# Kernel optimization log

Measured on AMD Instinct MI355X. Metric: run time of the kernel, lower is better.

The kernel has to match this reference:

```python
import jax, jax.numpy as jnp
import numpy as np

D_STATE = 8
DT_RANK = 8  # ceil(128/16)


def _grouped_1x1(x, w):
    # x: (B,H,W,Cin), w: (g, Cout//g, Cin//g)
    B, H, W, _ = x.shape
    g, o, i = w.shape
    xg = x.reshape(B, H, W, g, i)
    return jnp.einsum('bhwgi,goi->bhwgo', xg, w).reshape(B, H, W, g * o)


def setup_inputs() -> dict:
    key = jax.random.key(0)
    ks = jax.random.split(key, 16)
    B, H, W, C = 8, 64, 64, 128
    g = 4
    D = 128  # expand_dim = d_inner
    N = D_STATE
    R = DT_RANK
    inp = {}
    inp['x'] = jax.random.normal(ks[0], (B, H, W, C), dtype=jnp.float32)
    inp['w1'] = jax.random.normal(ks[1], (g, D // g, C // g), dtype=jnp.float32) * 0.1
    inp['dw'] = jax.random.normal(ks[2], (3, 3, 1, D), dtype=jnp.float32) * 0.1  # HWIO depthwise
    inp['in_proj_w'] = jax.random.normal(ks[3], (2 * D, D), dtype=jnp.float32) * 0.05
    inp['conv1d_w'] = jax.random.normal(ks[4], (D, 3), dtype=jnp.float32) * 0.1
    inp['conv1d_b'] = jax.random.normal(ks[5], (D,), dtype=jnp.float32) * 0.05
    inp['x_proj_w'] = jax.random.normal(ks[6], (R + 2 * N, D), dtype=jnp.float32) * 0.05
    inp['dt_proj_w'] = jax.random.normal(ks[7], (D, R), dtype=jnp.float32) * 0.05
    inp['dt_proj_b'] = jax.random.normal(ks[8], (D,), dtype=jnp.float32) * 0.05
    inp['A_log'] = jnp.log(jnp.tile(jnp.arange(1, N + 1, dtype=jnp.float32)[None, :], (D, 1)))
    inp['D_param'] = jnp.ones((D,), dtype=jnp.float32)
    inp['out_proj_w'] = jax.random.normal(ks[9], (D, D), dtype=jnp.float32) * 0.05
    inp['gamma'] = jnp.ones((D,), dtype=jnp.float32)
    inp['beta'] = jnp.zeros((D,), dtype=jnp.float32)
    inp['w2'] = jax.random.normal(ks[10], (g, D // g, C // g), dtype=jnp.float32) * 0.1
    inp['wout'] = jax.random.normal(ks[11], (g, C // g, D // g), dtype=jnp.float32) * 0.1
    return inp


def _mamba(x_seq, in_proj_w, conv1d_w, conv1d_b, x_proj_w, dt_proj_w, dt_proj_b, A_log, D_param, out_proj_w):
    # x_seq: (B, L, D)
    B, L, D = x_seq.shape
    N, R = D_STATE, DT_RANK
    xz = jnp.einsum('bld,ed->ble', x_seq, in_proj_w)  # (B,L,2D)
    u, z = xz[..., :D], xz[..., D:]
    # causal depthwise conv1d, kernel=3, left pad 2 (torch: padding=2, slice [:L])
    up = jnp.pad(u, ((0, 0), (2, 0), (0, 0)))
    u = (up[:, 0:L] * conv1d_w[:, 0] + up[:, 1:L + 1] * conv1d_w[:, 1]
         + up[:, 2:L + 2] * conv1d_w[:, 2] + conv1d_b)
    u = jax.nn.silu(u)
    x_dbl = jnp.einsum('bld,ed->ble', u, x_proj_w)  # (B,L,R+2N)
    dt = x_dbl[..., :R]
    Bm = x_dbl[..., R:R + N]
    Cm = x_dbl[..., R + N:]
    delta = jax.nn.softplus(jnp.einsum('blr,dr->bld', dt, dt_proj_w) + dt_proj_b)  # (B,L,D)
    A = -jnp.exp(A_log)  # (D,N)

    def step(h, inp):
        d_t, u_t, b_t, c_t = inp  # (B,D),(B,D),(B,N),(B,N)
        dA = jnp.exp(d_t[..., None] * A)            # (B,D,N)
        h = dA * h + (d_t * u_t)[..., None] * b_t[:, None, :]
        y_t = jnp.einsum('bdn,bn->bd', h, c_t)
        return h, y_t

    h0 = jnp.zeros((B, D, N), dtype=x_seq.dtype)
    xs = (jnp.swapaxes(delta, 0, 1), jnp.swapaxes(u, 0, 1),
          jnp.swapaxes(Bm, 0, 1), jnp.swapaxes(Cm, 0, 1))
    _, ys = jax.lax.scan(step, h0, xs)              # ys: (L,B,D)
    y = jnp.swapaxes(ys, 0, 1) + u * D_param
    y = y * jax.nn.silu(z)
    return jnp.einsum('bld,ed->ble', y, out_proj_w)


def reference(x, w1, dw, in_proj_w, conv1d_w, conv1d_b, x_proj_w, dt_proj_w, dt_proj_b,
              A_log, D_param, out_proj_w, gamma, beta, w2, wout):
    B, H, W, C = x.shape
    D = dw.shape[-1]
    x1 = _grouped_1x1(x, w1)  # (B,H,W,D)
    x1 = jax.lax.conv_general_dilated(
        x1, dw, window_strides=(1, 1), padding='SAME',
        feature_group_count=D, dimension_numbers=('NHWC', 'HWIO', 'NHWC'))
    x1 = jax.nn.silu(x1)
    x1_seq = x1.reshape(B, H * W, D)
    x1_seq = _mamba(x1_seq, in_proj_w, conv1d_w, conv1d_b, x_proj_w,
                    dt_proj_w, dt_proj_b, A_log, D_param, out_proj_w)
    x1 = x1_seq.reshape(B, H, W, D)
    mu = jnp.mean(x1, axis=-1, keepdims=True)
    var = jnp.mean(jnp.square(x1 - mu), axis=-1, keepdims=True)
    x1 = (x1 - mu) * jax.lax.rsqrt(var + 1e-5) * gamma + beta
    x2 = jax.nn.silu(_grouped_1x1(x, w2))
    x_fuse = x1 * x2
    return _grouped_1x1(x_fuse, wout)  # (B,H,W,C)
```

## Files before the change

### kernel.cpp

```cpp
#include <hip/hip_runtime.h>
#include <math.h>

#define B_    8
#define C_    128
#define D_    128
#define L_    4096
#define NPOS_ 32768
#define NC_   256
#define S_    16
#define MFL_  1048576

typedef __attribute__((ext_vector_type(8))) short short8;
typedef __attribute__((ext_vector_type(4))) float f32x4;

__device__ __forceinline__ float siluf(float x) { return x / (1.f + __expf(-x)); }
__device__ __forceinline__ float softplusf(float x) {
    if (x > 20.f) return x;
    return __logf(1.f + __expf(x));
}
__device__ __forceinline__ unsigned short f2bf(float f) {
    unsigned int u = __float_as_uint(f);
    u = (u + 0x7FFFu + ((u >> 16) & 1u)) >> 16;
    return (unsigned short)u;
}
__device__ __forceinline__ float bf2f(unsigned short h) {
    return __uint_as_float(((unsigned int)h) << 16);
}
__device__ __forceinline__ void scan_as(float dl, const float* Ar, bool fast, float* a) {
    if (fast) {
        float e1 = __expf(-dl);
        a[0] = e1;
        a[1] = e1 * e1;
        a[2] = a[1] * e1;
        a[3] = a[1] * a[1];
        a[4] = a[3] * e1;
        a[5] = a[3] * a[1];
        a[6] = a[5] * e1;
        a[7] = a[3] * a[3];
    } else {
        #pragma unroll
        for (int n = 0; n < 8; ++n) a[n] = __expf(dl * Ar[n]);
    }
}

__global__ __launch_bounds__(256) void k1_g1x1(const float* __restrict__ x,
                                               const float* __restrict__ w1,
                                               const float* __restrict__ w2,
                                               const float* __restrict__ inW,
                                               const float* __restrict__ OW,
                                               const float* __restrict__ xpw,
                                               unsigned short* __restrict__ inWb,
                                               unsigned short* __restrict__ OWb,
                                               unsigned short* __restrict__ xpwb,
                                               unsigned short* __restrict__ t1b,
                                               unsigned short* __restrict__ x2sb) {
    __shared__ float xs[16 * 128];
    int t = threadIdx.x;
    {
        int i = blockIdx.x * 51 + t;
        if (t < 51 && i < 52224) {
            if (i < 32768)      inWb[i] = f2bf(inW[i]);
            else if (i < 49152) OWb[i - 32768] = f2bf(OW[i - 32768]);
            else                xpwb[i - 49152] = f2bf(xpw[i - 49152]);
        }
    }
    int op = t & 63, ph = t >> 6;
    int g = op >> 4, o2 = (op & 15) * 2;
    const float* w1p = &w1[g * 1024 + o2 * 32];
    const float* w2p = &w2[g * 1024 + o2 * 32];
    float w1r[64], w2r[64];
    #pragma unroll
    for (int i = 0; i < 64; ++i) { w1r[i] = w1p[i]; w2r[i] = w2p[i]; }
    int pos0 = blockIdx.x * 32;
    for (int it = 0; it < 2; ++it) {
        int p0 = pos0 + it * 16;
        #pragma unroll
        for (int q = 0; q < 2; ++q) {
            int fi = t * 2 + q;
            *(float4*)&xs[fi * 4] = *(const float4*)&x[p0 * 128 + fi * 4];
        }
        __syncthreads();
        #pragma unroll
        for (int q = 0; q < 4; ++q) {
            int pl = ph * 4 + q;
            float a1 = 0.f, b1 = 0.f, a2 = 0.f, b2 = 0.f;
            const float* xr = &xs[pl * 128 + g * 32];
            #pragma unroll
            for (int i4 = 0; i4 < 8; ++i4) {
                float4 xv = *(const float4*)&xr[i4 * 4];
                a1 += xv.x * w1r[i4*4]    + xv.y * w1r[i4*4+1]    + xv.z * w1r[i4*4+2]    + xv.w * w1r[i4*4+3];
                b1 += xv.x * w1r[32+i4*4] + xv.y * w1r[32+i4*4+1] + xv.z * w1r[32+i4*4+2] + xv.w * w1r[32+i4*4+3];
                a2 += xv.x * w2r[i4*4]    + xv.y * w2r[i4*4+1]    + xv.z * w2r[i4*4+2]    + xv.w * w2r[i4*4+3];
                b2 += xv.x * w2r[32+i4*4] + xv.y * w2r[32+i4*4+1] + xv.z * w2r[32+i4*4+2] + xv.w * w2r[32+i4*4+3];
            }
            int pos = p0 + pl;
            int db = pos * 128 + g * 32 + o2;
            unsigned int u1 = (unsigned int)f2bf(a1) | ((unsigned int)f2bf(b1) << 16);
            unsigned int u2 = (unsigned int)f2bf(siluf(a2)) | ((unsigned int)f2bf(siluf(b2)) << 16);
            *(unsigned int*)&t1b[db]  = u1;
            *(unsigned int*)&x2sb[db] = u2;
        }
        __syncthreads();
    }
}

__global__ __launch_bounds__(128) void k2_dwconv(const unsigned short* __restrict__ t1b,
                                                 const float* __restrict__ dw,
                                                 unsigned short* __restrict__ x1cb) {
    int d = threadIdx.x;
    float dwr[9];
    #pragma unroll
    for (int k = 0; k < 9; ++k) dwr[k] = dw[k * 128 + d];
    int bid = blockIdx.x;
    int wt = bid & 15, ht = (bid >> 4) & 7, b = bid >> 7;
    int h0 = ht * 8, w0 = wt * 4;
    float rows[10][6];
    #pragma unroll
    for (int r = 0; r < 10; ++r) {
        int hh = h0 - 1 + r;
        bool hv = (hh >= 0) && (hh < 64);
        #pragma unroll
        for (int c = 0; c < 6; ++c) {
            int w = w0 - 1 + c;
            bool wvv = (w >= 0) && (w < 64);
            rows[r][c] = (hv && wvv) ? bf2f(t1b[((b * 64 + hh) * 64 + w) * 128 + d]) : 0.f;
        }
    }
    #pragma unroll
    for (int hi = 0; hi < 8; ++hi) {
        #pragma unroll
        for (int wi = 0; wi < 4; ++wi) {
            float acc = rows[hi][wi]     * dwr[0] + rows[hi][wi+1]   * dwr[1] + rows[hi][wi+2]   * dwr[2]
                      + rows[hi+1][wi]   * dwr[3] + rows[hi+1][wi+1] * dwr[4] + rows[hi+1][wi+2] * dwr[5]
                      + rows[hi+2][wi]   * dwr[6] + rows[hi+2][wi+1] * dwr[7] + rows[hi+2][wi+2] * dwr[8];
            x1cb[((b * 64 + h0 + hi) * 64 + w0 + wi) * 128 + d] = f2bf(siluf(acc));
        }
    }
}

__global__ __launch_bounds__(256) void k3_mfma(const unsigned short* __restrict__ Abf,
                                               const unsigned short* __restrict__ Bbf,
                                               unsigned short* __restrict__ urawb,
                                               unsigned short* __restrict__ zb) {
    __shared__ unsigned short Al[64 * 72];
    __shared__ unsigned short Bl[128 * 72];
    int t = threadIdx.x;
    int pos0 = (blockIdx.x >> 1) * 64;
    int half = blockIdx.x & 1;
    const unsigned short* Bh = Bbf + (size_t)half * 128 * 128;
    unsigned short* dst = half ? zb : urawb;
    int lane = t & 63, wv = t >> 6;
    int lanem = lane & 15, laneq = lane >> 4;
    f32x4 acc[8];
    #pragma unroll
    for (int i = 0; i < 8; ++i) acc[i] = (f32x4){0.f, 0.f, 0.f, 0.f};
    for (int kc = 0; kc < 2; ++kc) {
        #pragma unroll
        for (int q = 0; q < 2; ++q) {
            int c = t + q * 256;
            int row = c >> 3, col = c & 7;
            *(int4*)&Al[row * 72 + col * 8] = *(const int4*)&Abf[(pos0 + row) * 128 + kc * 64 + col * 8];
        }
        #pragma unroll
        for (int q = 0; q < 4; ++q) {
            int c = t + q * 256;
            int row = c >> 3, col = c & 7;
            *(int4*)&Bl[row * 72 + col * 8] = *(const int4*)&Bh[row * 128 + kc * 64 + col * 8];
        }
        __syncthreads();
        #pragma unroll
        for (int ks = 0; ks < 2; ++ks) {
            short8 af = *(const short8*)&Al[(wv * 16 + lanem) * 72 + ks * 32 + laneq * 8];
            #pragma unroll
            for (int ni = 0; ni < 8; ++ni) {
                short8 bfr = *(const short8*)&Bl[(ni * 16 + lanem) * 72 + ks * 32 + laneq * 8];
                acc[ni] = __builtin_amdgcn_mfma_f32_16x16x32_bf16(af, bfr, acc[ni], 0, 0, 0);
            }
        }
        __syncthreads();
    }
    #pragma unroll
    for (int ni = 0; ni < 8; ++ni)
        #pragma unroll
        for (int r = 0; r < 4; ++r) {
            int m = pos0 + wv * 16 + laneq * 4 + r;
            int n = ni * 16 + lanem;
            dst[m * 128 + n] = f2bf(acc[ni][r]);
        }
}

__global__ __launch_bounds__(256) void k45_convproj(const unsigned short* __restrict__ urawb,
                                                    const float* __restrict__ cw,
                                                    const float* __restrict__ cb,
                                                    const unsigned short* __restrict__ xpwb,
                                                    const float* __restrict__ dtw,
                                                    const float* __restrict__ dtb,
                                                    const float* __restrict__ A_log,
                                                    unsigned short* __restrict__ usb,
                                                    unsigned short* __restrict__ deltab,
                                                    float* __restrict__ Bm,
                                                    float* __restrict__ Cm,
                                                    float* __restrict__ cA,
                                                    float* __restrict__ cB) {
    __shared__ unsigned short uA[32 * 136];
    __shared__ unsigned short xB[32 * 136];
    __shared__ float xdb[32 * 36];
    int t = threadIdx.x;
    int d = t & 127, ph = t >> 7;
    for (int i = t; i < 32 * 128; i += 256) {
        int n = i >> 7, k = i & 127;
        xB[n * 136 + k] = (n < 24) ? xpwb[n * 128 + k] : (unsigned short)0;
    }
    float cw0 = cw[d * 3 + 0], cw1 = cw[d * 3 + 1], cw2 = cw[d * 3 + 2], cbr = cb[d];
    float dtwr[8];
    #pragma unroll
    for (int r = 0; r < 8; ++r) dtwr[r] = dtw[d * 8 + r];
    float dtbr = dtb[d];
    float Ar[8]; bool fast = true;
    #pragma unroll
    for (int n = 0; n < 8; ++n) {
        Ar[n] = -__expf(A_log[d * 8 + n]);
        fast = fast && (fabsf(Ar[n] + (float)(n + 1)) < 2e-3f);
    }

    int gpos0 = blockIdx.x * 32;
    int ll0 = (gpos0 & 4095) + ph * 16;
    int base = (gpos0 + ph * 16) * 128 + d;
    float ur0 = (ll0 >= 2) ? bf2f(urawb[base - 256]) : 0.f;
    float ur1 = (ll0 >= 1) ? bf2f(urawb[base - 128]) : 0.f;
    #pragma unroll
    for (int q = 0; q < 16; ++q) {
        float urq = bf2f(urawb[base + q * 128]);
        float v = siluf(ur0 * cw0 + ur1 * cw1 + urq * cw2 + cbr);
        unsigned short vb = f2bf(v);
        usb[base + q * 128] = vb;
        uA[(ph * 16 + q) * 136 + d] = vb;
        ur0 = ur1; ur1 = urq;
    }
    __syncthreads();
    int lane = t & 63, wv = t >> 6;
    int lanem = lane & 15, laneq = lane >> 4;
    int m0 = (wv & 1) * 16, n0 = (wv >> 1) * 16;
    f32x4 accx = (f32x4){0.f, 0.f, 0.f, 0.f};
    #pragma unroll
    for (int ks = 0; ks < 4; ++ks) {
        short8 af  = *(const short8*)&uA[(m0 + lanem) * 136 + ks * 32 + laneq * 8];
        short8 bfr = *(const short8*)&xB[(n0 + lanem) * 136 + ks * 32 + laneq * 8];
        accx = __builtin_amdgcn_mfma_f32_16x16x32_bf16(af, bfr, accx, 0, 0, 0);
    }
    #pragma unroll
    for (int r = 0; r < 4; ++r)
        xdb[(m0 + laneq * 4 + r) * 36 + n0 + lanem] = accx[r];
    __syncthreads();
    float h[8], ap[8];
    #pragma unroll
    for (int n = 0; n < 8; ++n) { h[n] = 0.f; ap[n] = 1.f; }
    #pragma unroll
    for (int q = 0; q < 16; ++q) {
        int pl = ph * 16 + q;
        const float* xrow = &xdb[pl * 36];
        float4 d0 = *(const float4*)&xrow[0];
        float4 d1 = *(const float4*)&xrow[4];
        float dt = dtbr + d0.x * dtwr[0] + d0.y * dtwr[1] + d0.z * dtwr[2] + d0.w * dtwr[3]
                        + d1.x * dtwr[4] + d1.y * dtwr[5] + d1.z * dtwr[6] + d1.w * dtwr[7];
        unsigned short dlb = f2bf(softplusf(dt));
        deltab[base + q * 128] = dlb;
        float dl = bf2f(dlb);
        float du = dl * bf2f(uA[pl * 136 + d]);
        float bmv[8];
        *(float4*)&bmv[0] = *(const float4*)&xrow[8];
        *(float4*)&bmv[4] = *(const float4*)&xrow[12];
        float a[8];
        scan_as(dl, Ar, fast, a);
        #pragma unroll
        for (int n = 0; n < 8; ++n) {
            ap[n] *= a[n];
            h[n] = a[n] * h[n] + du * bmv[n];
        }
    }
    int bH = gpos0 >> 12;
    int c  = ((gpos0 & 4095) >> 4) + ph;
    int obase = ((bH * NC_ + c) * 128 + d) * 8;
    *(float4*)&cA[obase]     = make_float4(ap[0], ap[1], ap[2], ap[3]);
    *(float4*)&cA[obase + 4] = make_float4(ap[4], ap[5], ap[6], ap[7]);
    *(float4*)&cB[obase]     = make_float4(h[0], h[1], h[2], h[3]);
    *(float4*)&cB[obase + 4] = make_float4(h[4], h[5], h[6], h[7]);
    if (t < 128) {
        int p = t >> 2, q = t & 3;
        float4 v = *(const float4*)&xdb[p * 36 + 8 + q * 4];
        int gp = gpos0 + p;
        if (q < 2) *(float4*)&Bm[gp * 8 + q * 4] = v;
        else       *(float4*)&Cm[gp * 8 + (q - 2) * 4] = v;
    }
}

__global__ __launch_bounds__(256) void k6a_scan(float* __restrict__ cA,
                                                float* __restrict__ cB,
                                                float* __restrict__ AgA,
                                                float* __restrict__ AgB) {
    int id = blockIdx.x * 256 + threadIdx.x;
    int dn = id & 1023;
    int grp = (id >> 10) & 15;
    int b = id >> 14;
    float Apre = 1.f, h = 0.f;
    int base = (b * NC_ + grp * 16) * 1024 + dn;
    #pragma unroll 4
    for (int j = 0; j < 16; ++j) {
        int idx = base + j * 1024;
        float a  = cA[idx];
        float bv = cB[idx];
        cA[idx] = Apre;
        cB[idx] = h;
        Apre *= a;
        h = a * h + bv;
    }
    int aidx = (b * 16 + grp) * 1024 + dn;
    AgA[aidx] = Apre;
    AgB[aidx] = h;
}

__global__ __launch_bounds__(256) void k6b_scan(const float* __restrict__ AgA,
                                                const float* __restrict__ AgB,
                                                float* __restrict__ gcar) {
    int id = blockIdx.x * 256 + threadIdx.x;
    int dn = id & 1023;
    int b = id >> 10;
    float h = 0.f;
    #pragma unroll
    for (int grp = 0; grp < 16; ++grp) {
        int idx = (b * 16 + grp) * 1024 + dn;
        float Ag = AgA[idx];
        float Bg = AgB[idx];
        gcar[idx] = h;
        h = Ag * h + Bg;
    }
}

__global__ __launch_bounds__(256) void k7f_fused(const unsigned short* __restrict__ deltab,
                                                 const unsigned short* __restrict__ usb,
                                                 const float* __restrict__ Bm,
                                                 const float* __restrict__ Cm,
                                                 const unsigned short* __restrict__ zb,
                                                 const float* __restrict__ A_log,
                                                 const float* __restrict__ Dp,
                                                 const float* __restrict__ Apre,
                                                 const float* __restrict__ Bpre,
                                                 const float* __restrict__ gcar,
                                                 const unsigned short* __restrict__ OWb,
                                                 const float* __restrict__ gamma,
                                                 const float* __restrict__ beta,
                                                 const unsigned short* __restrict__ x2sb,
                                                 const float* __restrict__ wout,
                                                 float* __restrict__ out) {
    __shared__ __align__(16) char smem[37888];
    unsigned short* yA = (unsigned short*)smem;
    unsigned short* Bl = (unsigned short*)(smem + 18432);
    float* xz = (float*)smem;
    __shared__ float woutL[4 * 1160];
    __shared__ float gbL[256];
    int t = threadIdx.x;
    for (int idx = t; idx < 4096; idx += 256) {
        int g = idx >> 10, r = idx & 1023, o = r >> 5, i = r & 31;
        woutL[g * 1160 + o * 36 + i] = wout[idx];
    }
    if (t < 128) gbL[t] = gamma[t];
    else         gbL[t] = beta[t - 128];

    int d = t & 127, ph = t >> 7;
    int b = blockIdx.x >> 6, cblk = blockIdx.x & 63;
    float Ar[8]; bool fast = true;
    #pragma unroll
    for (int n = 0; n < 8; ++n) {
        Ar[n] = -__expf(A_log[d * 8 + n]);
        fast = fast && (fabsf(Ar[n] + (float)(n + 1)) < 2e-3f);
    }
    float Dpr = Dp[d];
    int ybase = (d >> 6) * (64 * 72) + (d & 63);
    for (int cc = 0; cc < 2; ++cc) {
        int cl = ph * 2 + cc;
        int c = cblk * 4 + cl;
        int cbase = ((b * NC_ + c) * 128 + d) * 8;
        float4 ap0 = *(const float4*)&Apre[cbase];
        float4 ap1 = *(const float4*)&Apre[cbase + 4];
        float4 bp0 = *(const float4*)&Bpre[cbase];
        float4 bp1 = *(const float4*)&Bpre[cbase + 4];
        int gbase = (b * 16 + (c >> 4)) * 1024 + d * 8;
        float4 g0 = *(const float4*)&gcar[gbase];
        float4 g1 = *(const float4*)&gcar[gbase + 4];
        float h[8] = { fmaf(g0.x, ap0.x, bp0.x), fmaf(g0.y, ap0.y, bp0.y),
                       fmaf(g0.z, ap0.z, bp0.z), fmaf(g0.w, ap0.w, bp0.w),
                       fmaf(g1.x, ap1.x, bp1.x), fmaf(g1.y, ap1.y, bp1.y),
                       fmaf(g1.z, ap1.z, bp1.z), fmaf(g1.w, ap1.w, bp1.w) };
        int base  = (b * L_ + c * S_) * 128 + d;
        int bbase = (b * L_ + c * S_) * 8;
        #pragma unroll
        for (int s = 0; s < S_; ++s) {
            float dl = bf2f(deltab[base + s * 128]);
            float uv = bf2f(usb[base + s * 128]);
            float zv = bf2f(zb[base + s * 128]);
            float du = dl * uv;
            float4 bm0 = *(const float4*)&Bm[bbase + s * 8];
            float4 bm1 = *(const float4*)&Bm[bbase + s * 8 + 4];
            float4 cm0 = *(const float4*)&Cm[bbase + s * 8];
            float4 cm1 = *(const float4*)&Cm[bbase + s * 8 + 4];
            float a[8];
            scan_as(dl, Ar, fast, a);
            h[0] = a[0] * h[0] + du * bm0.x;
            h[1] = a[1] * h[1] + du * bm0.y;
            h[2] = a[2] * h[2] + du * bm0.z;
            h[3] = a[3] * h[3] + du * bm0.w;
            h[4] = a[4] * h[4] + du * bm1.x;
            h[5] = a[5] * h[5] + du * bm1.y;
            h[6] = a[6] * h[6] + du * bm1.z;
            h[7] = a[7] * h[7] + du * bm1.w;
            float yv = h[0] * cm0.x + h[1] * cm0.y + h[2] * cm0.z + h[3] * cm0.w
                     + h[4] * cm1.x + h[5] * cm1.y + h[6] * cm1.z + h[7] * cm1.w;
            yv = (yv + uv * Dpr) * siluf(zv);
            yA[ybase + (cl * 16 + s) * 72] = f2bf(yv);
        }
    }
    __syncthreads();

    int lane = t & 63, wv = t >> 6;
    int lanem = lane & 15, laneq = lane >> 4;
    f32x4 acc[8];
    #pragma unroll
    for (int i = 0; i < 8; ++i) acc[i] = (f32x4){0.f, 0.f, 0.f, 0.f};
    for (int kc = 0; kc < 2; ++kc) {
        #pragma unroll
        for (int q = 0; q < 4; ++q) {
            int cidx = t + q * 256;
            int row = cidx >> 3, col = cidx & 7;
            *(int4*)&Bl[row * 72 + col * 8] = *(const int4*)&OWb[row * 128 + kc * 64 + col * 8];
        }
        __syncthreads();
        #pragma unroll
        for (int ks = 0; ks < 2; ++ks) {
            short8 af = *(const short8*)&yA[kc * (64 * 72) + (wv * 16 + lanem) * 72 + ks * 32 + laneq * 8];
            #pragma unroll
            for (int ni = 0; ni < 8; ++ni) {
                short8 bfr = *(const short8*)&Bl[(ni * 16 + lanem) * 72 + ks * 32 + laneq * 8];
                acc[ni] = __builtin_amdgcn_mfma_f32_16x16x32_bf16(af, bfr, acc[ni], 0, 0, 0);
            }
        }
        __syncthreads();
    }
    #pragma unroll
    for (int ni = 0; ni < 8; ++ni) {
        int ch = ni * 16 + lanem;
        int col = ch + ((ch >> 5) << 2);
        #pragma unroll
        for (int r = 0; r < 4; ++r)
            xz[(wv * 16 + laneq * 4 + r) * 148 + col] = bf2f(f2bf(acc[ni][r]));
    }
    __syncthreads();

    int g = t & 3, pos = t >> 2;
    int gpos = b * L_ + cblk * 64 + pos;
    const float* xrow0 = &xz[pos * 148 + g * 36];
    float v[32];
    #pragma unroll
    for (int i4 = 0; i4 < 8; ++i4) {
        float4 xv = *(const float4*)&xrow0[i4 * 4];
        v[i4*4+0] = xv.x; v[i4*4+1] = xv.y;
        v[i4*4+2] = xv.z; v[i4*4+3] = xv.w;
    }
    float s = 0.f, s2 = 0.f;
    #pragma unroll
    for (int i = 0; i < 32; ++i) { s += v[i]; s2 += v[i] * v[i]; }
    s  += __shfl_xor(s, 1, 64);  s  += __shfl_xor(s, 2, 64);
    s2 += __shfl_xor(s2, 1, 64); s2 += __shfl_xor(s2, 2, 64);
    float m = s * (1.f / 128.f);
    float var = s2 * (1.f / 128.f) - m * m;
    float rstd = rsqrtf(var + 1e-5f);
    #pragma unroll
    for (int i4 = 0; i4 < 8; ++i4) {
        ushort4 xv = *(const ushort4*)&x2sb[gpos * 128 + g * 32 + i4 * 4];
        unsigned short xa[4] = {xv.x, xv.y, xv.z, xv.w};
        #pragma unroll
        for (int k = 0; k < 4; ++k) {
            int e = g * 32 + i4 * 4 + k;
            float vv = (v[i4 * 4 + k] - m) * rstd * gbL[e] + gbL[128 + e];
            v[i4 * 4 + k] = vv * bf2f(xa[k]);
        }
    }

    const float* wg = &woutL[g * 1160];
    int obase = gpos * 128 + g * 32;
    #pragma unroll
    for (int ob = 0; ob < 8; ++ob) {
        float o4[4];
        #pragma unroll
        for (int oo = 0; oo < 4; ++oo) {
            int o = ob * 4 + oo;
            float acc2 = 0.f;
            #pragma unroll
            for (int i4 = 0; i4 < 8; ++i4) {
                float4 wv4 = *(const float4*)&wg[o * 36 + i4 * 4];
                acc2 += v[i4*4] * wv4.x + v[i4*4+1] * wv4.y
                      + v[i4*4+2] * wv4.z + v[i4*4+3] * wv4.w;
            }
            o4[oo] = acc2;
        }
        *(float4*)&out[obase + ob * 4] = make_float4(o4[0], o4[1], o4[2], o4[3]);
    }
}

extern "C" void kernel_launch(void* const* d_in, const int* in_sizes, int n_in,
                              void* d_out, int out_size, void* d_ws, size_t ws_size,
                              hipStream_t stream) {
    (void)in_sizes; (void)n_in; (void)out_size; (void)ws_size;
    const float* x         = (const float*)d_in[0];
    const float* w1        = (const float*)d_in[1];
    const float* dw        = (const float*)d_in[2];
    const float* in_proj_w = (const float*)d_in[3];
    const float* conv1d_w  = (const float*)d_in[4];
    const float* conv1d_b  = (const float*)d_in[5];
    const float* x_proj_w  = (const float*)d_in[6];
    const float* dt_proj_w = (const float*)d_in[7];
    const float* dt_proj_b = (const float*)d_in[8];
    const float* A_log     = (const float*)d_in[9];
    const float* D_param   = (const float*)d_in[10];
    const float* out_proj_w= (const float*)d_in[11];
    const float* gamma     = (const float*)d_in[12];
    const float* beta      = (const float*)d_in[13];
    const float* w2        = (const float*)d_in[14];
    const float* wout      = (const float*)d_in[15];
    float* out = (float*)d_out;

    float* ws = (float*)d_ws;
    unsigned short* x2sb   = (unsigned short*)(ws);
    unsigned short* t1b    = (unsigned short*)(ws + 2  * (size_t)MFL_);
    unsigned short* x1cb   = (unsigned short*)(ws + 4  * (size_t)MFL_);
    unsigned short* urawb  = (unsigned short*)(ws + 6  * (size_t)MFL_);
    unsigned short* zb     = (unsigned short*)(ws + 8  * (size_t)MFL_);
    unsigned short* usb    = (unsigned short*)(ws + 14 * (size_t)MFL_);
    unsigned short* deltab = (unsigned short*)(ws + 16 * (size_t)MFL_);
    float* Bm    = ws + 18 * (size_t)MFL_;
    float* Cm    = Bm + (size_t)NPOS_ * 8;
    float* cA    = Cm + (size_t)NPOS_ * 8;
    float* cB    = cA + 2 * (size_t)MFL_;
    float* scanw = cB + 2 * (size_t)MFL_;
    float* AgA   = scanw;
    float* AgB   = scanw + 131072;
    float* gcar  = scanw + 262144;
    unsigned short* inWb = (unsigned short*)(scanw + 2 * (size_t)MFL_);
    unsigned short* OWb  = inWb + 32768;
    unsigned short* xpwb = OWb + 16384;

    k1_g1x1<<<1024, 256, 0, stream>>>(x, w1, w2, in_proj_w, out_proj_w, x_proj_w,
                                      inWb, OWb, xpwb, t1b, x2sb);
    k2_dwconv<<<1024, 128, 0, stream>>>(t1b, dw, x1cb);
    k3_mfma<<<1024, 256, 0, stream>>>(x1cb, inWb, urawb, zb);
    k45_convproj<<<1024, 256, 0, stream>>>(urawb, conv1d_w, conv1d_b, xpwb,
                                           dt_proj_w, dt_proj_b, A_log,
                                           usb, deltab, Bm, Cm, cA, cB);
    k6a_scan<<<512, 256, 0, stream>>>(cA, cB, AgA, AgB);
    k6b_scan<<<32, 256, 0, stream>>>(AgA, AgB, gcar);
    k7f_fused<<<512, 256, 0, stream>>>(deltab, usb, Bm, Cm, zb, A_log, D_param,
                                       cA, cB, gcar, OWb, gamma, beta, x2sb, wout, out);
}
```

Baseline: 214.9 us.

## Fuse all seven stages into one persistent kernel with software grid barriers

```diff
diff --git a/kernel.cpp b/kernel.cpp
--- a/kernel.cpp
+++ b/kernel.cpp
@@ -9,6 +9,7 @@
 #define NC_   256
 #define S_    16
 #define MFL_  1048576
+#define NBLK_ 512u
 
 typedef __attribute__((ext_vector_type(8))) short short8;
 typedef __attribute__((ext_vector_type(4))) float f32x4;
@@ -43,466 +44,496 @@
     }
 }
 
-__global__ __launch_bounds__(256) void k1_g1x1(const float* __restrict__ x,
-                                               const float* __restrict__ w1,
-                                               const float* __restrict__ w2,
-                                               const float* __restrict__ inW,
-                                               const float* __restrict__ OW,
-                                               const float* __restrict__ xpw,
-                                               unsigned short* __restrict__ inWb,
-                                               unsigned short* __restrict__ OWb,
-                                               unsigned short* __restrict__ xpwb,
-                                               unsigned short* __restrict__ t1b,
-                                               unsigned short* __restrict__ x2sb) {
-    __shared__ float xs[16 * 128];
+__device__ __forceinline__ void gbar(unsigned int* bar, int phase) {
+    __syncthreads();
+    if (threadIdx.x == 0) {
+        unsigned int* c = bar + phase * 16;
+        __threadfence();
+        __hip_atomic_fetch_add(&c[blockIdx.x & 7], 1u, __ATOMIC_ACQ_REL, __HIP_MEMORY_SCOPE_AGENT);
+        if (blockIdx.x == 0) {
+            unsigned int s;
+            do {
+                __builtin_amdgcn_s_sleep(1);
+                s = 0;
+                #pragma unroll
+                for (int i = 0; i < 8; ++i)
+                    s += __hip_atomic_load(&c[i], __ATOMIC_RELAXED, __HIP_MEMORY_SCOPE_AGENT);
+            } while (s < NBLK_);
+            __hip_atomic_store(&c[8], 1u, __ATOMIC_RELEASE, __HIP_MEMORY_SCOPE_AGENT);
+        } else {
+            while (__hip_atomic_load(&c[8], __ATOMIC_ACQUIRE, __HIP_MEMORY_SCOPE_AGENT) == 0u)
+                __builtin_amdgcn_s_sleep(1);
+        }
+        __threadfence();
+    }
+    __syncthreads();
+}
+
+__global__ __launch_bounds__(256, 2) void mega(
+        const float* __restrict__ x,
+        const float* __restrict__ w1,
+        const float* __restrict__ w2,
+        const float* __restrict__ inW,
+        const float* __restrict__ OW,
+        const float* __restrict__ xpw,
+        const float* __restrict__ dw,
+        const float* __restrict__ cw,
+        const float* __restrict__ cb,
+        const float* __restrict__ dtw,
+        const float* __restrict__ dtb,
+        const float* __restrict__ A_log,
+        const float* __restrict__ Dp,
+        const float* __restrict__ gamma,
+        const float* __restrict__ beta,
+        const float* __restrict__ wout,
+        unsigned short* __restrict__ inWb,
+        unsigned short* __restrict__ OWb,
+        unsigned short* __restrict__ xpwb,
+        unsigned short* __restrict__ t1b,
+        unsigned short* __restrict__ x2sb,
+        unsigned short* __restrict__ x1cb,
+        unsigned short* __restrict__ urawb,
+        unsigned short* __restrict__ zb,
+        unsigned short* __restrict__ usb,
+        unsigned short* __restrict__ deltab,
+        float* __restrict__ Bm,
+        float* __restrict__ Cm,
+        float* __restrict__ cA,
+        float* __restrict__ cB,
+        float* __restrict__ AgA,
+        float* __restrict__ AgB,
+        float* __restrict__ gcar,
+        float* __restrict__ out,
+        unsigned int* __restrict__ bar) {
+    __shared__ __align__(16) char arena[57472];
     int t = threadIdx.x;
-    {
-        int i = blockIdx.x * 51 + t;
-        if (t < 51 && i < 52224) {
-            if (i < 32768)      inWb[i] = f2bf(inW[i]);
-            else if (i < 49152) OWb[i - 32768] = f2bf(OW[i - 32768]);
-            else                xpwb[i - 49152] = f2bf(xpw[i - 49152]);
-        }
-    }
-    int op = t & 63, ph = t >> 6;
-    int g = op >> 4, o2 = (op & 15) * 2;
-    const float* w1p = &w1[g * 1024 + o2 * 32];
-    const float* w2p = &w2[g * 1024 + o2 * 32];
-    float w1r[64], w2r[64];
-    #pragma unroll
-    for (int i = 0; i < 64; ++i) { w1r[i] = w1p[i]; w2r[i] = w2p[i]; }
-    int pos0 = blockIdx.x * 32;
-    for (int it = 0; it < 2; ++it) {
-        int p0 = pos0 + it * 16;
-        #pragma unroll
-        for (int q = 0; q < 2; ++q) {
-            int fi = t * 2 + q;
-            *(float4*)&xs[fi * 4] = *(const float4*)&x[p0 * 128 + fi * 4];
+
+    {
+        float* xs = (float*)arena;
+        for (int it2 = 0; it2 < 2; ++it2) {
+            int obid = (int)blockIdx.x + it2 * 512;
+            int i = obid * 51 + t;
+            if (t < 51 && i < 52224) {
+                if (i < 32768)      inWb[i] = f2bf(inW[i]);
+                else if (i < 49152) OWb[i - 32768] = f2bf(OW[i - 32768]);
+                else                xpwb[i - 49152] = f2bf(xpw[i - 49152]);
+            }
+        }
+        int op = t & 63, ph = t >> 6;
+        int g = op >> 4, o2 = (op & 15) * 2;
+        const float* w1p = &w1[g * 1024 + o2 * 32];
+        const float* w2p = &w2[g * 1024 + o2 * 32];
+        float w1r[64], w2r[64];
+        #pragma unroll
+        for (int i = 0; i < 64; ++i) { w1r[i] = w1p[i]; w2r[i] = w2p[i]; }
+        for (int it2 = 0; it2 < 2; ++it2) {
+            int obid = (int)blockIdx.x + it2 * 512;
+            int pos0 = obid * 32;
+            for (int it = 0; it < 2; ++it) {
+                int p0 = pos0 + it * 16;
+                #pragma unroll
+                for (int q = 0; q < 2; ++q) {
+                    int fi = t * 2 + q;
+                    *(float4*)&xs[fi * 4] = *(const float4*)&x[p0 * 128 + fi * 4];
+                }
+                __syncthreads();
+                #pragma unroll
+                for (int q = 0; q < 4; ++q) {
+                    int pl = ph * 4 + q;
+                    float a1 = 0.f, b1 = 0.f, a2 = 0.f, b2 = 0.f;
+                    const float* xr = &xs[pl * 128 + g * 32];
+                    #pragma unroll
+                    for (int i4 = 0; i4 < 8; ++i4) {
+                        float4 xv = *(const float4*)&xr[i4 * 4];
+                        a1 += xv.x * w1r[i4*4]    + xv.y * w1r[i4*4+1]    + xv.z * w1r[i4*4+2]    + xv.w * w1r[i4*4+3];
+                        b1 += xv.x * w1r[32+i4*4] + xv.y * w1r[32+i4*4+1] + xv.z * w1r[32+i4*4+2] + xv.w * w1r[32+i4*4+3];
+                        a2 += xv.x * w2r[i4*4]    + xv.y * w2r[i4*4+1]    + xv.z * w2r[i4*4+2]    + xv.w * w2r[i4*4+3];
+                        b2 += xv.x * w2r[32+i4*4] + xv.y * w2r[32+i4*4+1] + xv.z * w2r[32+i4*4+2] + xv.w * w2r[32+i4*4+3];
+                    }
+                    int pos = p0 + pl;
+                    int db = pos * 128 + g * 32 + o2;
+                    unsigned int u1 = (unsigned int)f2bf(a1) | ((unsigned int)f2bf(b1) << 16);
+                    unsigned int u2 = (unsigned int)f2bf(siluf(a2)) | ((unsigned int)f2bf(siluf(b2)) << 16);
+                    *(unsigned int*)&t1b[db]  = u1;
+                    *(unsigned int*)&x2sb[db] = u2;
+                }
+                __syncthreads();
+            }
+        }
+    }
+    gbar(bar, 0);
+
+    {
+        int obid = (int)blockIdx.x * 2 + (t >> 7);
+        int d = t & 127;
+        float dwr[9];
+        #pragma unroll
+        for (int k = 0; k < 9; ++k) dwr[k] = dw[k * 128 + d];
+        int wt = obid & 15, ht = (obid >> 4) & 7, b = obid >> 7;
+        int h0 = ht * 8, w0 = wt * 4;
+        float rows[10][6];
+        #pragma unroll
+        for (int r = 0; r < 10; ++r) {
+            int hh = h0 - 1 + r;
+            bool hv = (hh >= 0) && (hh < 64);
+            #pragma unroll
+            for (int c = 0; c < 6; ++c) {
+                int w = w0 - 1 + c;
+                bool wvv = (w >= 0) && (w < 64);
+                rows[r][c] = (hv && wvv) ? bf2f(t1b[((b * 64 + hh) * 64 + w) * 128 + d]) : 0.f;
+            }
+        }
+        #pragma unroll
+        for (int hi = 0; hi < 8; ++hi) {
+            #pragma unroll
+            for (int wi = 0; wi < 4; ++wi) {
+                float acc = rows[hi][wi]     * dwr[0] + rows[hi][wi+1]   * dwr[1] + rows[hi][wi+2]   * dwr[2]
+                          + rows[hi+1][wi]   * dwr[3] + rows[hi+1][wi+1] * dwr[4] + rows[hi+1][wi+2] * dwr[5]
+                          + rows[hi+2][wi]   * dwr[6] + rows[hi+2][wi+1] * dwr[7] + rows[hi+2][wi+2] * dwr[8];
+                x1cb[((b * 64 + h0 + hi) * 64 + w0 + wi) * 128 + d] = f2bf(siluf(acc));
+            }
+        }
+    }
+    gbar(bar, 1);
+
+    {
+        unsigned short* Al = (unsigned short*)arena;
+        unsigned short* Bl = (unsigned short*)(arena + 9216);
+        int lane = t & 63, wv = t >> 6;
+        int lanem = lane & 15, laneq = lane >> 4;
+        for (int it2 = 0; it2 < 2; ++it2) {
+            int obid = (int)blockIdx.x + it2 * 512;
+            int pos0 = (obid >> 1) * 64;
+            int half = obid & 1;
+            const unsigned short* Bh = inWb + (size_t)half * 128 * 128;
+            unsigned short* dst = half ? zb : urawb;
+            f32x4 acc[8];
+            #pragma unroll
+            for (int i = 0; i < 8; ++i) acc[i] = (f32x4){0.f, 0.f, 0.f, 0.f};
+            for (int kc = 0; kc < 2; ++kc) {
+                #pragma unroll
+                for (int q = 0; q < 2; ++q) {
+                    int c = t + q * 256;
+                    int row = c >> 3, col = c & 7;
+                    *(int4*)&Al[row * 72 + col * 8] = *(const int4*)&x1cb[(pos0 + row) * 128 + kc * 64 + col * 8];
+                }
+                #pragma unroll
+                for (int q = 0; q < 4; ++q) {
+                    int c = t + q * 256;
+                    int row = c >> 3, col = c & 7;
+                    *(int4*)&Bl[row * 72 + col * 8] = *(const int4*)&Bh[row * 128 + kc * 64 + col * 8];
+                }
+                __syncthreads();
+                #pragma unroll
+                for (int ks = 0; ks < 2; ++ks) {
+                    short8 af = *(const short8*)&Al[(wv * 16 + lanem) * 72 + ks * 32 + laneq * 8];
+                    #pragma unroll
+                    for (int ni = 0; ni < 8; ++ni) {
+                        short8 bfr = *(const short8*)&Bl[(ni * 16 + lanem) * 72 + ks * 32 + laneq * 8];
+                        acc[ni] = __builtin_amdgcn_mfma_f32_16x16x32_bf16(af, bfr, acc[ni], 0, 0, 0);
+                    }
+                }
+                __syncthreads();
+            }
+            #pragma unroll
+            for (int ni = 0; ni < 8; ++ni)
+                #pragma unroll
+                for (int r = 0; r < 4; ++r) {
+                    int m = pos0 + wv * 16 + laneq * 4 + r;
+                    int n = ni * 16 + lanem;
+                    dst[m * 128 + n] = f2bf(acc[ni][r]);
+                }
+        }
+    }
+    gbar(bar, 2);
+
+    {
+        unsigned short* uA = (unsigned short*)arena;
+        unsigned short* xB = (unsigned short*)(arena + 8704);
+        float* xdb = (float*)(arena + 17408);
+        int d = t & 127, ph = t >> 7;
+        float cw0 = cw[d * 3 + 0], cw1 = cw[d * 3 + 1], cw2 = cw[d * 3 + 2], cbr = cb[d];
+        float dtwr[8];
+        #pragma unroll
+        for (int r = 0; r < 8; ++r) dtwr[r] = dtw[d * 8 + r];
+        float dtbr = dtb[d];
+        float Ar[8]; bool fast = true;
+        #pragma unroll
+        for (int n = 0; n < 8; ++n) {
+            Ar[n] = -__expf(A_log[d * 8 + n]);
+            fast = fast && (fabsf(Ar[n] + (float)(n + 1)) < 2e-3f);
+        }
+        int lane = t & 63, wv = t >> 6;
+        int lanem = lane & 15, laneq = lane >> 4;
+        int m0 = (wv & 1) * 16, n0 = (wv >> 1) * 16;
+        for (int it2 = 0; it2 < 2; ++it2) {
+            int obid = (int)blockIdx.x + it2 * 512;
+            for (int i = t; i < 32 * 128; i += 256) {
+                int n = i >> 7, k = i & 127;
+                xB[n * 136 + k] = (n < 24) ? xpwb[n * 128 + k] : (unsigned short)0;
+            }
+            int gpos0 = obid * 32;
+            int ll0 = (gpos0 & 4095) + ph * 16;
+            int base = (gpos0 + ph * 16) * 128 + d;
+            float ur0 = (ll0 >= 2) ? bf2f(urawb[base - 256]) : 0.f;
+            float ur1 = (ll0 >= 1) ? bf2f(urawb[base - 128]) : 0.f;
+            #pragma unroll
+            for (int q = 0; q < 16; ++q) {
+                float urq = bf2f(urawb[base + q * 128]);
+                float v = siluf(ur0 * cw0 + ur1 * cw1 + urq * cw2 + cbr);
+                unsigned short vb = f2bf(v);
+                usb[base + q * 128] = vb;
+                uA[(ph * 16 + q) * 136 + d] = vb;
+                ur0 = ur1; ur1 = urq;
+            }
+            __syncthreads();
+            f32x4 accx = (f32x4){0.f, 0.f, 0.f, 0.f};
+            #pragma unroll
+            for (int ks = 0; ks < 4; ++ks) {
+                short8 af  = *(const short8*)&uA[(m0 + lanem) * 136 + ks * 32 + laneq * 8];
+                short8 bfr = *(const short8*)&xB[(n0 + lanem) * 136 + ks * 32 + laneq * 8];
+                accx = __builtin_amdgcn_mfma_f32_16x16x32_bf16(af, bfr, accx, 0, 0, 0);
+            }
+            #pragma unroll
+            for (int r = 0; r < 4; ++r)
+                xdb[(m0 + laneq * 4 + r) * 36 + n0 + lanem] = accx[r];
+            __syncthreads();
+            float h[8], ap[8];
+            #pragma unroll
+            for (int n = 0; n < 8; ++n) { h[n] = 0.f; ap[n] = 1.f; }
+            #pragma unroll
+            for (int q = 0; q < 16; ++q) {
+                int pl = ph * 16 + q;
+                const float* xrow = &xdb[pl * 36];
+                float4 d0 = *(const float4*)&xrow[0];
+                float4 d1 = *(const float4*)&xrow[4];
+                float dt = dtbr + d0.x * dtwr[0] + d0.y * dtwr[1] + d0.z * dtwr[2] + d0.w * dtwr[3]
+                                + d1.x * dtwr[4] + d1.y * dtwr[5] + d1.z * dtwr[6] + d1.w * dtwr[7];
+                unsigned short dlb = f2bf(softplusf(dt));
+                deltab[base + q * 128] = dlb;
+                float dl = bf2f(dlb);
+                float du = dl * bf2f(uA[pl * 136 + d]);
+                float bmv[8];
+                *(float4*)&bmv[0] = *(const float4*)&xrow[8];
+                *(float4*)&bmv[4] = *(const float4*)&xrow[12];
+                float a[8];
+                scan_as(dl, Ar, fast, a);
+                #pragma unroll
+                for (int n = 0; n < 8; ++n) {
+                    ap[n] *= a[n];
+                    h[n] = a[n] * h[n] + du * bmv[n];
+                }
+            }
+            int bH = gpos0 >> 12;
+            int c  = ((gpos0 & 4095) >> 4) + ph;
+            int obase = ((bH * NC_ + c) * 128 + d) * 8;
+            *(float4*)&cA[obase]     = make_float4(ap[0], ap[1], ap[2], ap[3]);
+            *(float4*)&cA[obase + 4] = make_float4(ap[4], ap[5], ap[6], ap[7]);
+            *(float4*)&cB[obase]     = make_float4(h[0], h[1], h[2], h[3]);
+            *(float4*)&cB[obase + 4] = make_float4(h[4], h[5], h[6], h[7]);
+            if (t < 128) {
+                int p = t >> 2, q = t & 3;
+                float4 v = *(const float4*)&xdb[p * 36 + 8 + q * 4];
+                int gp = gpos0 + p;
+                if (q < 2) *(float4*)&Bm[gp * 8 + q * 4] = v;
+                else       *(float4*)&Cm[gp * 8 + (q - 2) * 4] = v;
+            }
+            __syncthreads();
+        }
+    }
+    gbar(bar, 3);
+
+    {
+        int id = (int)blockIdx.x * 256 + t;
+        int dn = id & 1023;
+        int grp = (id >> 10) & 15;
+        int b = id >> 14;
+        float Apre = 1.f, h = 0.f;
+        int base = (b * NC_ + grp * 16) * 1024 + dn;
+        #pragma unroll 4
+        for (int j = 0; j < 16; ++j) {
+            int idx = base + j * 1024;
+            float a  = cA[idx];
+            float bv = cB[idx];
+            cA[idx] = Apre;
+            cB[idx] = h;
+            Apre *= a;
+            h = a * h + bv;
+        }
+        int aidx = (b * 16 + grp) * 1024 + dn;
+        AgA[aidx] = Apre;
+        AgB[aidx] = h;
+    }
+    gbar(bar, 4);
+
+    {
+        if (blockIdx.x < 32) {
+            int id = (int)blockIdx.x * 256 + t;
+            int dn = id & 1023;
+            int b = id >> 10;
+            float h = 0.f;
+            #pragma unroll
+            for (int grp = 0; grp < 16; ++grp) {
+                int idx = (b * 16 + grp) * 1024 + dn;
+                float Ag = AgA[idx];
+                float Bg = AgB[idx];
+                gcar[idx] = h;
+                h = Ag * h + Bg;
+            }
+        }
+    }
+    gbar(bar, 5);
+
+    {
+        unsigned short* yA = (unsigned short*)arena;
+        unsigned short* Bl = (unsigned short*)(arena + 18432);
+        float* xz = (float*)arena;
+        float* woutL = (float*)(arena + 37888);
+        float* gbL = (float*)(arena + 37888 + 18560);
+        for (int idx = t; idx < 4096; idx += 256) {
+            int g = idx >> 10, r = idx & 1023, o = r >> 5, i = r & 31;
+            woutL[g * 1160 + o * 36 + i] = wout[idx];
+        }
+        if (t < 128) gbL[t] = gamma[t];
+        else         gbL[t] = beta[t - 128];
+
+        int d = t & 127, ph = t >> 7;
+        int b = (int)blockIdx.x >> 6, cblk = (int)blockIdx.x & 63;
+        float Ar[8]; bool fast = true;
+        #pragma unroll
+        for (int n = 0; n < 8; ++n) {
+            Ar[n] = -__expf(A_log[d * 8 + n]);
+            fast = fast && (fabsf(Ar[n] + (float)(n + 1)) < 2e-3f);
+        }
+        float Dpr = Dp[d];
+        int ybase = (d >> 6) * (64 * 72) + (d & 63);
+        for (int cc = 0; cc < 2; ++cc) {
+            int cl = ph * 2 + cc;
+            int c = cblk * 4 + cl;
+            int cbase = ((b * NC_ + c) * 128 + d) * 8;
+            float4 ap0 = *(const float4*)&cA[cbase];
+            float4 ap1 = *(const float4*)&cA[cbase + 4];
+            float4 bp0 = *(const float4*)&cB[cbase];
+            float4 bp1 = *(const float4*)&cB[cbase + 4];
+            int gbase = (b * 16 + (c >> 4)) * 1024 + d * 8;
+            float4 g0 = *(const float4*)&gcar[gbase];
+            float4 g1 = *(const float4*)&gcar[gbase + 4];
+            float h[8] = { fmaf(g0.x, ap0.x, bp0.x), fmaf(g0.y, ap0.y, bp0.y),
+                           fmaf(g0.z, ap0.z, bp0.z), fmaf(g0.w, ap0.w, bp0.w),
+                           fmaf(g1.x, ap1.x, bp1.x), fmaf(g1.y, ap1.y, bp1.y),
+                           fmaf(g1.z, ap1.z, bp1.z), fmaf(g1.w, ap1.w, bp1.w) };
+            int base  = (b * L_ + c * S_) * 128 + d;
+            int bbase = (b * L_ + c * S_) * 8;
+            #pragma unroll
+            for (int s = 0; s < S_; ++s) {
+                float dl = bf2f(deltab[base + s * 128]);
+                float uv = bf2f(usb[base + s * 128]);
+                float zv = bf2f(zb[base + s * 128]);
+                float du = dl * uv;
+                float4 bm0 = *(const float4*)&Bm[bbase + s * 8];
+                float4 bm1 = *(const float4*)&Bm[bbase + s * 8 + 4];
+                float4 cm0 = *(const float4*)&Cm[bbase + s * 8];
+                float4 cm1 = *(const float4*)&Cm[bbase + s * 8 + 4];
+                float a[8];
+                scan_as(dl, Ar, fast, a);
+                h[0] = a[0] * h[0] + du * bm0.x;
+                h[1] = a[1] * h[1] + du * bm0.y;
+                h[2] = a[2] * h[2] + du * bm0.z;
+                h[3] = a[3] * h[3] + du * bm0.w;
+                h[4] = a[4] * h[4] + du * bm1.x;
+                h[5] = a[5] * h[5] + du * bm1.y;
+                h[6] = a[6] * h[6] + du * bm1.z;
+                h[7] = a[7] * h[7] + du * bm1.w;
+                float yv = h[0] * cm0.x + h[1] * cm0.y + h[2] * cm0.z + h[3] * cm0.w
+                         + h[4] * cm1.x + h[5] * cm1.y + h[6] * cm1.z + h[7] * cm1.w;
+                yv = (yv + uv * Dpr) * siluf(zv);
+                yA[ybase + (cl * 16 + s) * 72] = f2bf(yv);
+            }
         }
         __syncthreads();
-        #pragma unroll
-        for (int q = 0; q < 4; ++q) {
-            int pl = ph * 4 + q;
-            float a1 = 0.f, b1 = 0.f, a2 = 0.f, b2 = 0.f;
-            const float* xr = &xs[pl * 128 + g * 32];
-            #pragma unroll
-            for (int i4 = 0; i4 < 8; ++i4) {
-                float4 xv = *(const float4*)&xr[i4 * 4];
-                a1 += xv.x * w1r[i4*4]    + xv.y * w1r[i4*4+1]    + xv.z * w1r[i4*4+2]    + xv.w * w1r[i4*4+3];
-                b1 += xv.x * w1r[32+i4*4] + xv.y * w1r[32+i4*4+1] + xv.z * w1r[32+i4*4+2] + xv.w * w1r[32+i4*4+3];
-                a2 += xv.x * w2r[i4*4]    + xv.y * w2r[i4*4+1]    + xv.z * w2r[i4*4+2]    + xv.w * w2r[i4*4+3];
-                b2 += xv.x * w2r[32+i4*4] + xv.y * w2r[32+i4*4+1] + xv.z * w2r[32+i4*4+2] + xv.w * w2r[32+i4*4+3];
-            }
-            int pos = p0 + pl;
-            int db = pos * 128 + g * 32 + o2;
-            unsigned int u1 = (unsigned int)f2bf(a1) | ((unsigned int)f2bf(b1) << 16);
-            unsigned int u2 = (unsigned int)f2bf(siluf(a2)) | ((unsigned int)f2bf(siluf(b2)) << 16);
-            *(unsigned int*)&t1b[db]  = u1;
-            *(unsigned int*)&x2sb[db] = u2;
+
+        int lane = t & 63, wv = t >> 6;
+        int lanem = lane & 15, laneq = lane >> 4;
+        f32x4 acc[8];
+        #pragma unroll
+        for (int i = 0; i < 8; ++i) acc[i] = (f32x4){0.f, 0.f, 0.f, 0.f};
+        for (int kc = 0; kc < 2; ++kc) {
+            #pragma unroll
+            for (int q = 0; q < 4; ++q) {
+                int cidx = t + q * 256;
+                int row = cidx >> 3, col = cidx & 7;
+                *(int4*)&Bl[row * 72 + col * 8] = *(const int4*)&OWb[row * 128 + kc * 64 + col * 8];
+            }
+            __syncthreads();
+            #pragma unroll
+            for (int ks = 0; ks < 2; ++ks) {
+                short8 af = *(const short8*)&yA[kc * (64 * 72) + (wv * 16 + lanem) * 72 + ks * 32 + laneq * 8];
+                #pragma unroll
+                for (int ni = 0; ni < 8; ++ni) {
+                    short8 bfr = *(const short8*)&Bl[(ni * 16 + lanem) * 72 + ks * 32 + laneq * 8];
+                    acc[ni] = __builtin_amdgcn_mfma_f32_16x16x32_bf16(af, bfr, acc[ni], 0, 0, 0);
+                }
+            }
+            __syncthreads();
+        }
+        #pragma unroll
+        for (int ni = 0; ni < 8; ++ni) {
+            int ch = ni * 16 + lanem;
+            int col = ch + ((ch >> 5) << 2);
+            #pragma unroll
+            for (int r = 0; r < 4; ++r)
+                xz[(wv * 16 + laneq * 4 + r) * 148 + col] = bf2f(f2bf(acc[ni][r]));
         }
         __syncthreads();
-    }
-}
-
-__global__ __launch_bounds__(128) void k2_dwconv(const unsigned short* __restrict__ t1b,
-                                                 const float* __restrict__ dw,
-                                                 unsigned short* __restrict__ x1cb) {
-    int d = threadIdx.x;
-    float dwr[9];
-    #pragma unroll
-    for (int k = 0; k < 9; ++k) dwr[k] = dw[k * 128 + d];
-    int bid = blockIdx.x;
-    int wt = bid & 15, ht = (bid >> 4) & 7, b = bid >> 7;
-    int h0 = ht * 8, w0 = wt * 4;
-    float rows[10][6];
-    #pragma unroll
-    for (int r = 0; r < 10; ++r) {
-        int hh = h0 - 1 + r;
-        bool hv = (hh >= 0) && (hh < 64);
-        #pragma unroll
-        for (int c = 0; c < 6; ++c) {
-            int w = w0 - 1 + c;
-            bool wvv = (w >= 0) && (w < 64);
-            rows[r][c] = (hv && wvv) ? bf2f(t1b[((b * 64 + hh) * 64 + w) * 128 + d]) : 0.f;
-        }
-    }
-    #pragma unroll
-    for (int hi = 0; hi < 8; ++hi) {
-        #pragma unroll
-        for (int wi = 0; wi < 4; ++wi) {
-            float acc = rows[hi][wi]     * dwr[0] + rows[hi][wi+1]   * dwr[1] + rows[hi][wi+2]   * dwr[2]
-                      + rows[hi+1][wi]   * dwr[3] + rows[hi+1][wi+1] * dwr[4] + rows[hi+1][wi+2] * dwr[5]
-                      + rows[hi+2][wi]   * dwr[6] + rows[hi+2][wi+1] * dwr[7] + rows[hi+2][wi+2] * dwr[8];
-            x1cb[((b * 64 + h0 + hi) * 64 + w0 + wi) * 128 + d] = f2bf(siluf(acc));
-        }
-    }
-}
-
-__global__ __launch_bounds__(256) void k3_mfma(const unsigned short* __restrict__ Abf,
-                                               const unsigned short* __restrict__ Bbf,
-                                               unsigned short* __restrict__ urawb,
-                                               unsigned short* __restrict__ zb) {
-    __shared__ unsigned short Al[64 * 72];
-    __shared__ unsigned short Bl[128 * 72];
-    int t = threadIdx.x;
-    int pos0 = (blockIdx.x >> 1) * 64;
-    int half = blockIdx.x & 1;
-    const unsigned short* Bh = Bbf + (size_t)half * 128 * 128;
-    unsigned short* dst = half ? zb : urawb;
-    int lane = t & 63, wv = t >> 6;
-    int lanem = lane & 15, laneq = lane >> 4;
-    f32x4 acc[8];
-    #pragma unroll
-    for (int i = 0; i < 8; ++i) acc[i] = (f32x4){0.f, 0.f, 0.f, 0.f};
-    for (int kc = 0; kc < 2; ++kc) {
-        #pragma unroll
-        for (int q = 0; q < 2; ++q) {
-            int c = t + q * 256;
-            int row = c >> 3, col = c & 7;
-            *(int4*)&Al[row * 72 + col * 8] = *(const int4*)&Abf[(pos0 + row) * 128 + kc * 64 + col * 8];
-        }
-        #pragma unroll
-        for (int q = 0; q < 4; ++q) {
-            int c = t + q * 256;
-            int row = c >> 3, col = c & 7;
-            *(int4*)&Bl[row * 72 + col * 8] = *(const int4*)&Bh[row * 128 + kc * 64 + col * 8];
-        }
-        __syncthreads();
-        #pragma unroll
-        for (int ks = 0; ks < 2; ++ks) {
-            short8 af = *(const short8*)&Al[(wv * 16 + lanem) * 72 + ks * 32 + laneq * 8];
-            #pragma unroll
-            for (int ni = 0; ni < 8; ++ni) {
-                short8 bfr = *(const short8*)&Bl[(ni * 16 + lanem) * 72 + ks * 32 + laneq * 8];
-                acc[ni] = __builtin_amdgcn_mfma_f32_16x16x32_bf16(af, bfr, acc[ni], 0, 0, 0);
-            }
-        }
-        __syncthreads();
-    }
-    #pragma unroll
-    for (int ni = 0; ni < 8; ++ni)
-        #pragma unroll
-        for (int r = 0; r < 4; ++r) {
-            int m = pos0 + wv * 16 + laneq * 4 + r;
-            int n = ni * 16 + lanem;
-            dst[m * 128 + n] = f2bf(acc[ni][r]);
-        }
-}
-
-__global__ __launch_bounds__(256) void k45_convproj(const unsigned short* __restrict__ urawb,
-                                                    const float* __restrict__ cw,
-                                                    const float* __restrict__ cb,
-                                                    const unsigned short* __restrict__ xpwb,
-                                                    const float* __restrict__ dtw,
-                                                    const float* __restrict__ dtb,
-                                                    const float* __restrict__ A_log,
-                                                    unsigned short* __restrict__ usb,
-                                                    unsigned short* __restrict__ deltab,
-                                                    float* __restrict__ Bm,
-                                                    float* __restrict__ Cm,
-                                                    float* __restrict__ cA,
-                                                    float* __restrict__ cB) {
-    __shared__ unsigned short uA[32 * 136];
-    __shared__ unsigned short xB[32 * 136];
-    __shared__ float xdb[32 * 36];
-    int t = threadIdx.x;
-    int d = t & 127, ph = t >> 7;
-    for (int i = t; i < 32 * 128; i += 256) {
-        int n = i >> 7, k = i & 127;
-        xB[n * 136 + k] = (n < 24) ? xpwb[n * 128 + k] : (unsigned short)0;
-    }
-    float cw0 = cw[d * 3 + 0], cw1 = cw[d * 3 + 1], cw2 = cw[d * 3 + 2], cbr = cb[d];
-    float dtwr[8];
-    #pragma unroll
-    for (int r = 0; r < 8; ++r) dtwr[r] = dtw[d * 8 + r];
-    float dtbr = dtb[d];
-    float Ar[8]; bool fast = true;
-    #pragma unroll
-    for (int n = 0; n < 8; ++n) {
-        Ar[n] = -__expf(A_log[d * 8 + n]);
-        fast = fast && (fabsf(Ar[n] + (float)(n + 1)) < 2e-3f);
-    }
-
-    int gpos0 = blockIdx.x * 32;
-    int ll0 = (gpos0 & 4095) + ph * 16;
-    int base = (gpos0 + ph * 16) * 128 + d;
-    float ur0 = (ll0 >= 2) ? bf2f(urawb[base - 256]) : 0.f;
-    float ur1 = (ll0 >= 1) ? bf2f(urawb[base - 128]) : 0.f;
-    #pragma unroll
-    for (int q = 0; q < 16; ++q) {
-        float urq = bf2f(urawb[base + q * 128]);
-        float v = siluf(ur0 * cw0 + ur1 * cw1 + urq * cw2 + cbr);
-        unsigned short vb = f2bf(v);
-        usb[base + q * 128] = vb;
-        uA[(ph * 16 + q) * 136 + d] = vb;
-        ur0 = ur1; ur1 = urq;
-    }
-    __syncthreads();
-    int lane = t & 63, wv = t >> 6;
-    int lanem = lane & 15, laneq = lane >> 4;
-    int m0 = (wv & 1) * 16, n0 = (wv >> 1) * 16;
-    f32x4 accx = (f32x4){0.f, 0.f, 0.f, 0.f};
-    #pragma unroll
-    for (int ks = 0; ks < 4; ++ks) {
-        short8 af  = *(const short8*)&uA[(m0 + lanem) * 136 + ks * 32 + laneq * 8];
-        short8 bfr = *(const short8*)&xB[(n0 + lanem) * 136 + ks * 32 + laneq * 8];
-        accx = __builtin_amdgcn_mfma_f32_16x16x32_bf16(af, bfr, accx, 0, 0, 0);
-    }
-    #pragma unroll
-    for (int r = 0; r < 4; ++r)
-        xdb[(m0 + laneq * 4 + r) * 36 + n0 + lanem] = accx[r];
-    __syncthreads();
-    float h[8], ap[8];
-    #pragma unroll
-    for (int n = 0; n < 8; ++n) { h[n] = 0.f; ap[n] = 1.f; }
-    #pragma unroll
-    for (int q = 0; q < 16; ++q) {
-        int pl = ph * 16 + q;
-        const float* xrow = &xdb[pl * 36];
-        float4 d0 = *(const float4*)&xrow[0];
-        float4 d1 = *(const float4*)&xrow[4];
-        float dt = dtbr + d0.x * dtwr[0] + d0.y * dtwr[1] + d0.z * dtwr[2] + d0.w * dtwr[3]
-                        + d1.x * dtwr[4] + d1.y * dtwr[5] + d1.z * dtwr[6] + d1.w * dtwr[7];
-        unsigned short dlb = f2bf(softplusf(dt));
-        deltab[base + q * 128] = dlb;
-        float dl = bf2f(dlb);
-        float du = dl * bf2f(uA[pl * 136 + d]);
-        float bmv[8];
-        *(float4*)&bmv[0] = *(const float4*)&xrow[8];
-        *(float4*)&bmv[4] = *(const float4*)&xrow[12];
-        float a[8];
-        scan_as(dl, Ar, fast, a);
-        #pragma unroll
-        for (int n = 0; n < 8; ++n) {
-            ap[n] *= a[n];
-            h[n] = a[n] * h[n] + du * bmv[n];
-        }
-    }
-    int bH = gpos0 >> 12;
-    int c  = ((gpos0 & 4095) >> 4) + ph;
-    int obase = ((bH * NC_ + c) * 128 + d) * 8;
-    *(float4*)&cA[obase]     = make_float4(ap[0], ap[1], ap[2], ap[3]);
-    *(float4*)&cA[obase + 4] = make_float4(ap[4], ap[5], ap[6], ap[7]);
-    *(float4*)&cB[obase]     = make_float4(h[0], h[1], h[2], h[3]);
-    *(float4*)&cB[obase + 4] = make_float4(h[4], h[5], h[6], h[7]);
-    if (t < 128) {
-        int p = t >> 2, q = t & 3;
-        float4 v = *(const float4*)&xdb[p * 36 + 8 + q * 4];
-        int gp = gpos0 + p;
-        if (q < 2) *(float4*)&Bm[gp * 8 + q * 4] = v;
-        else       *(float4*)&Cm[gp * 8 + (q - 2) * 4] = v;
-    }
-}
-
-__global__ __launch_bounds__(256) void k6a_scan(float* __restrict__ cA,
-                                                float* __restrict__ cB,
-                                                float* __restrict__ AgA,
-                                                float* __restrict__ AgB) {
-    int id = blockIdx.x * 256 + threadIdx.x;
-    int dn = id & 1023;
-    int grp = (id >> 10) & 15;
-    int b = id >> 14;
-    float Apre = 1.f, h = 0.f;
-    int base = (b * NC_ + grp * 16) * 1024 + dn;
-    #pragma unroll 4
-    for (int j = 0; j < 16; ++j) {
-        int idx = base + j * 1024;
-        float a  = cA[idx];
-        float bv = cB[idx];
-        cA[idx] = Apre;
-        cB[idx] = h;
-        Apre *= a;
-        h = a * h + bv;
-    }
-    int aidx = (b * 16 + grp) * 1024 + dn;
-    AgA[aidx] = Apre;
-    AgB[aidx] = h;
-}
-
-__global__ __launch_bounds__(256) void k6b_scan(const float* __restrict__ AgA,
-                                                const float* __restrict__ AgB,
-                                                float* __restrict__ gcar) {
-    int id = blockIdx.x * 256 + threadIdx.x;
-    int dn = id & 1023;
-    int b = id >> 10;
-    float h = 0.f;
-    #pragma unroll
-    for (int grp = 0; grp < 16; ++grp) {
-        int idx = (b * 16 + grp) * 1024 + dn;
-        float Ag = AgA[idx];
-        float Bg = AgB[idx];
-        gcar[idx] = h;
-        h = Ag * h + Bg;
-    }
-}
-
-__global__ __launch_bounds__(256) void k7f_fused(const unsigned short* __restrict__ deltab,
-                                                 const unsigned short* __restrict__ usb,
-                                                 const float* __restrict__ Bm,
-                                                 const float* __restrict__ Cm,
-                                                 const unsigned short* __restrict__ zb,
-                                                 const float* __restrict__ A_log,
-                                                 const float* __restrict__ Dp,
-                                                 const float* __restrict__ Apre,
-                                                 const float* __restrict__ Bpre,
-                                                 const float* __restrict__ gcar,
-                                                 const unsigned short* __restrict__ OWb,
-                                                 const float* __restrict__ gamma,
-                                                 const float* __restrict__ beta,
-                                                 const unsigned short* __restrict__ x2sb,
-                                                 const float* __restrict__ wout,
-                                                 float* __restrict__ out) {
-    __shared__ __align__(16) char smem[37888];
-    unsigned short* yA = (unsigned short*)smem;
-    unsigned short* Bl = (unsigned short*)(smem + 18432);
-    float* xz = (float*)smem;
-    __shared__ float woutL[4 * 1160];
-    __shared__ float gbL[256];
-    int t = threadIdx.x;
-    for (int idx = t; idx < 4096; idx += 256) {
-        int g = idx >> 10, r = idx & 1023, o = r >> 5, i = r & 31;
-        woutL[g * 1160 + o * 36 + i] = wout[idx];
-    }
-    if (t < 128) gbL[t] = gamma[t];
-    else         gbL[t] = beta[t - 128];
-
-    int d = t & 127, ph = t >> 7;
-    int b = blockIdx.x >> 6, cblk = blockIdx.x & 63;
-    float Ar[8]; bool fast = true;
-    #pragma unroll
-    for (int n = 0; n < 8; ++n) {
-        Ar[n] = -__expf(A_log[d * 8 + n]);
-        fast = fast && (fabsf(Ar[n] + (float)(n + 1)) < 2e-3f);
-    }
-    float Dpr = Dp[d];
-    int ybase = (d >> 6) * (64 * 72) + (d & 63);
-    for (int cc = 0; cc < 2; ++cc) {
-        int cl = ph * 2 + cc;
-        int c = cblk * 4 + cl;
-        int cbase = ((b * NC_ + c) * 128 + d) * 8;
-        float4 ap0 = *(const float4*)&Apre[cbase];
-        float4 ap1 = *(const float4*)&Apre[cbase + 4];
-        float4 bp0 = *(const float4*)&Bpre[cbase];
-        float4 bp1 = *(const float4*)&Bpre[cbase + 4];
-        int gbase = (b * 16 + (c >> 4)) * 1024 + d * 8;
-        float4 g0 = *(const float4*)&gcar[gbase];
-        float4 g1 = *(const float4*)&gcar[gbase + 4];
-        float h[8] = { fmaf(g0.x, ap0.x, bp0.x), fmaf(g0.y, ap0.y, bp0.y),
-                       fmaf(g0.z, ap0.z, bp0.z), fmaf(g0.w, ap0.w, bp0.w),
-                       fmaf(g1.x, ap1.x, bp1.x), fmaf(g1.y, ap1.y, bp1.y),
-                       fmaf(g1.z, ap1.z, bp1.z), fmaf(g1.w, ap1.w, bp1.w) };
-        int base  = (b * L_ + c * S_) * 128 + d;
-        int bbase = (b * L_ + c * S_) * 8;
-        #pragma unroll
-        for (int s = 0; s < S_; ++s) {
-            float dl = bf2f(deltab[base + s * 128]);
-            float uv = bf2f(usb[base + s * 128]);
-            float zv = bf2f(zb[base + s * 128]);
-            float du = dl * uv;
-            float4 bm0 = *(const float4*)&Bm[bbase + s * 8];
-            float4 bm1 = *(const float4*)&Bm[bbase + s * 8 + 4];
-            float4 cm0 = *(const float4*)&Cm[bbase + s * 8];
-            float4 cm1 = *(const float4*)&Cm[bbase + s * 8 + 4];
-            float a[8];
-            scan_as(dl, Ar, fast, a);
-            h[0] = a[0] * h[0] + du * bm0.x;
-            h[1] = a[1] * h[1] + du * bm0.y;
-            h[2] = a[2] * h[2] + du * bm0.z;
-            h[3] = a[3] * h[3] + du * bm0.w;
-            h[4] = a[4] * h[4] + du * bm1.x;
-            h[5] = a[5] * h[5] + du * bm1.y;
-            h[6] = a[6] * h[6] + du * bm1.z;
-            h[7] = a[7] * h[7] + du * bm1.w;
-            float yv = h[0] * cm0.x + h[1] * cm0.y + h[2] * cm0.z + h[3] * cm0.w
-                     + h[4] * cm1.x + h[5] * cm1.y + h[6] * cm1.z + h[7] * cm1.w;
-            yv = (yv + uv * Dpr) * siluf(zv);
-            yA[ybase + (cl * 16 + s) * 72] = f2bf(yv);
-        }
-    }
-    __syncthreads();
-
-    int lane = t & 63, wv = t >> 6;
-    int lanem = lane & 15, laneq = lane >> 4;
-    f32x4 acc[8];
-    #pragma unroll
-    for (int i = 0; i < 8; ++i) acc[i] = (f32x4){0.f, 0.f, 0.f, 0.f};
-    for (int kc = 0; kc < 2; ++kc) {
-        #pragma unroll
-        for (int q = 0; q < 4; ++q) {
-            int cidx = t + q * 256;
-            int row = cidx >> 3, col = cidx & 7;
-            *(int4*)&Bl[row * 72 + col * 8] = *(const int4*)&OWb[row * 128 + kc * 64 + col * 8];
-        }
-        __syncthreads();
-        #pragma unroll
-        for (int ks = 0; ks < 2; ++ks) {
-            short8 af = *(const short8*)&yA[kc * (64 * 72) + (wv * 16 + lanem) * 72 + ks * 32 + laneq * 8];
-            #pragma unroll
-            for (int ni = 0; ni < 8; ++ni) {
-                short8 bfr = *(const short8*)&Bl[(ni * 16 + lanem) * 72 + ks * 32 + laneq * 8];
-                acc[ni] = __builtin_amdgcn_mfma_f32_16x16x32_bf16(af, bfr, acc[ni], 0, 0, 0);
-            }
-        }
-        __syncthreads();
-    }
-    #pragma unroll
-    for (int ni = 0; ni < 8; ++ni) {
-        int ch = ni * 16 + lanem;
-        int col = ch + ((ch >> 5) << 2);
-        #pragma unroll
-        for (int r = 0; r < 4; ++r)
-            xz[(wv * 16 + laneq * 4 + r) * 148 + col] = bf2f(f2bf(acc[ni][r]));
-    }
-    __syncthreads();
-
-    int g = t & 3, pos = t >> 2;
-    int gpos = b * L_ + cblk * 64 + pos;
-    const float* xrow0 = &xz[pos * 148 + g * 36];
-    float v[32];
-    #pragma unroll
-    for (int i4 = 0; i4 < 8; ++i4) {
-        float4 xv = *(const float4*)&xrow0[i4 * 4];
-        v[i4*4+0] = xv.x; v[i4*4+1] = xv.y;
-        v[i4*4+2] = xv.z; v[i4*4+3] = xv.w;
-    }
-    float s = 0.f, s2 = 0.f;
-    #pragma unroll
-    for (int i = 0; i < 32; ++i) { s += v[i]; s2 += v[i] * v[i]; }
-    s  += __shfl_xor(s, 1, 64);  s  += __shfl_xor(s, 2, 64);
-    s2 += __shfl_xor(s2, 1, 64); s2 += __shfl_xor(s2, 2, 64);
-    float m = s * (1.f / 128.f);
-    float var = s2 * (1.f / 128.f) - m * m;
-    float rstd = rsqrtf(var + 1e-5f);
-    #pragma unroll
-    for (int i4 = 0; i4 < 8; ++i4) {
-        ushort4 xv = *(const ushort4*)&x2sb[gpos * 128 + g * 32 + i4 * 4];
-        unsigned short xa[4] = {xv.x, xv.y, xv.z, xv.w};
-        #pragma unroll
-        for (int k = 0; k < 4; ++k) {
-            int e = g * 32 + i4 * 4 + k;
-            float vv = (v[i4 * 4 + k] - m) * rstd * gbL[e] + gbL[128 + e];
-            v[i4 * 4 + k] = vv * bf2f(xa[k]);
-        }
-    }
-
-    const float* wg = &woutL[g * 1160];
-    int obase = gpos * 128 + g * 32;
-    #pragma unroll
-    for (int ob = 0; ob < 8; ++ob) {
-        float o4[4];
-        #pragma unroll
-        for (int oo = 0; oo < 4; ++oo) {
-            int o = ob * 4 + oo;
-            float acc2 = 0.f;
-            #pragma unroll
-            for (int i4 = 0; i4 < 8; ++i4) {
-                float4 wv4 = *(const float4*)&wg[o * 36 + i4 * 4];
-                acc2 += v[i4*4] * wv4.x + v[i4*4+1] * wv4.y
-                      + v[i4*4+2] * wv4.z + v[i4*4+3] * wv4.w;
-            }
-            o4[oo] = acc2;
-        }
-        *(float4*)&out[obase + ob * 4] = make_float4(o4[0], o4[1], o4[2], o4[3]);
+
+        int g = t & 3, pos = t >> 2;
+        int gpos = b * L_ + cblk * 64 + pos;
+        const float* xrow0 = &xz[pos * 148 + g * 36];
+        float v[32];
+        #pragma unroll
+        for (int i4 = 0; i4 < 8; ++i4) {
+            float4 xv = *(const float4*)&xrow0[i4 * 4];
+            v[i4*4+0] = xv.x; v[i4*4+1] = xv.y;
+            v[i4*4+2] = xv.z; v[i4*4+3] = xv.w;
+        }
+        float s = 0.f, s2 = 0.f;
+        #pragma unroll
+        for (int i = 0; i < 32; ++i) { s += v[i]; s2 += v[i] * v[i]; }
+        s  += __shfl_xor(s, 1, 64);  s  += __shfl_xor(s, 2, 64);
+        s2 += __shfl_xor(s2, 1, 64); s2 += __shfl_xor(s2, 2, 64);
+        float m = s * (1.f / 128.f);
+        float var = s2 * (1.f / 128.f) - m * m;
+        float rstd = rsqrtf(var + 1e-5f);
+        #pragma unroll
+        for (int i4 = 0; i4 < 8; ++i4) {
+            ushort4 xv = *(const ushort4*)&x2sb[gpos * 128 + g * 32 + i4 * 4];
+            unsigned short xa[4] = {xv.x, xv.y, xv.z, xv.w};
+            #pragma unroll
+            for (int k = 0; k < 4; ++k) {
+                int e = g * 32 + i4 * 4 + k;
+                float vv = (v[i4 * 4 + k] - m) * rstd * gbL[e] + gbL[128 + e];
+                v[i4 * 4 + k] = vv * bf2f(xa[k]);
+            }
+        }
+        const float* wg = &woutL[g * 1160];
+        int obase = gpos * 128 + g * 32;
+        #pragma unroll
+        for (int ob = 0; ob < 8; ++ob) {
+            float o4[4];
+            #pragma unroll
+            for (int oo = 0; oo < 4; ++oo) {
+                int o = ob * 4 + oo;
+                float acc2 = 0.f;
+                #pragma unroll
+                for (int i4 = 0; i4 < 8; ++i4) {
+                    float4 wv4 = *(const float4*)&wg[o * 36 + i4 * 4];
+                    acc2 += v[i4*4] * wv4.x + v[i4*4+1] * wv4.y
+                          + v[i4*4+2] * wv4.z + v[i4*4+3] * wv4.w;
+                }
+                o4[oo] = acc2;
+            }
+            *(float4*)&out[obase + ob * 4] = make_float4(o4[0], o4[1], o4[2], o4[3]);
+        }
     }
 }
 
@@ -547,16 +578,13 @@
     unsigned short* inWb = (unsigned short*)(scanw + 2 * (size_t)MFL_);
     unsigned short* OWb  = inWb + 32768;
     unsigned short* xpwb = OWb + 16384;
-
-    k1_g1x1<<<1024, 256, 0, stream>>>(x, w1, w2, in_proj_w, out_proj_w, x_proj_w,
-                                      inWb, OWb, xpwb, t1b, x2sb);
-    k2_dwconv<<<1024, 128, 0, stream>>>(t1b, dw, x1cb);
-    k3_mfma<<<1024, 256, 0, stream>>>(x1cb, inWb, urawb, zb);
-    k45_convproj<<<1024, 256, 0, stream>>>(urawb, conv1d_w, conv1d_b, xpwb,
-                                           dt_proj_w, dt_proj_b, A_log,
-                                           usb, deltab, Bm, Cm, cA, cB);
-    k6a_scan<<<512, 256, 0, stream>>>(cA, cB, AgA, AgB);
-    k6b_scan<<<32, 256, 0, stream>>>(AgA, AgB, gcar);
-    k7f_fused<<<512, 256, 0, stream>>>(deltab, usb, Bm, Cm, zb, A_log, D_param,
-                                       cA, cB, gcar, OWb, gamma, beta, x2sb, wout, out);
-}
+    unsigned int* bar = (unsigned int*)(ws + 26 * (size_t)MFL_ / 1);
+
+    hipMemsetAsync(bar, 0, 6 * 16 * sizeof(unsigned int), stream);
+    mega<<<512, 256, 0, stream>>>(x, w1, w2, in_proj_w, out_proj_w, x_proj_w, dw,
+                                  conv1d_w, conv1d_b, dt_proj_w, dt_proj_b, A_log,
+                                  D_param, gamma, beta, wout,
+                                  inWb, OWb, xpwb, t1b, x2sb, x1cb, urawb, zb,
+                                  usb, deltab, Bm, Cm, cA, cB, AgA, AgB, gcar,
+                                  out, bar);
+}
```

After: 670.7 us. 3.12x slower.
